# Kernel tuning notes

Measured on AMD Instinct MI355X. Metric: run time of the kernel, lower is better.

Reference implementation:

```python
import jax, jax.numpy as jnp
import numpy as np

TEMP = 1.0
EPS = 1e-6


def trop_linear(x, w, b, temp=TEMP):
    # x: (..., in), w: (out, in) -> (..., out)
    # y_i = temp * logsumexp_j((w_ij + x_j)/temp) + b_i  (soft tropical / max-plus)
    z = x[..., None, :] + w  # (..., out, in)
    y = temp * jax.nn.logsumexp(z / temp, axis=-1)
    return y + b


def trop_layernorm(x, weight, bias, eps=EPS):
    n = x.shape[-1]
    # torch.median returns the lower of the two middle elements for even n
    med = jnp.sort(x, axis=-1)[..., (n - 1) // 2][..., None]
    q75 = jnp.quantile(x, 0.75, axis=-1, keepdims=True)
    q25 = jnp.quantile(x, 0.25, axis=-1, keepdims=True)
    iqr = jnp.maximum(q75 - q25, eps)
    return (x - med) / iqr * weight + bias


def setup_inputs() -> dict:
    key = jax.random.key(0)
    ks = jax.random.split(key, 8)
    B, D_IN, D_H, D_OUT = 1024, 512, 512, 256
    return {
        "x": jax.random.normal(ks[0], (B, D_IN), dtype=jnp.float32),
        "w1": 0.1 * jax.random.normal(ks[1], (D_H, D_IN), dtype=jnp.float32),
        "b1": jnp.zeros((D_H,), dtype=jnp.float32),
        "ln1_w": jnp.ones((D_H,), dtype=jnp.float32),
        "ln1_b": jnp.zeros((D_H,), dtype=jnp.float32),
        "w2": 0.1 * jax.random.normal(ks[2], (D_H, D_H), dtype=jnp.float32),
        "b2": jnp.zeros((D_H,), dtype=jnp.float32),
        "ln2_w": jnp.ones((D_H,), dtype=jnp.float32),
        "ln2_b": jnp.zeros((D_H,), dtype=jnp.float32),
        "w3": 0.1 * jax.random.normal(ks[3], (D_OUT, D_H), dtype=jnp.float32),
        "b3": jnp.zeros((D_OUT,), dtype=jnp.float32),
    }


def reference(x, w1, b1, ln1_w, ln1_b, w2, b2, ln2_w, ln2_b, w3, b3):
    h = trop_linear(x, w1, b1)
    h = trop_layernorm(h, ln1_w, ln1_b)
    h = jnp.maximum(h, 0.0)  # TropicalActivation('relu', threshold=0)
    h = trop_linear(h, w2, b2)
    h = trop_layernorm(h, ln2_w, ln2_b)
    h = jnp.maximum(h, 0.0)
    return trop_linear(h, w3, b3)
```

## Files before the change

kernel.cpp:

```cpp
#include <hip/hip_runtime.h>
#include <math.h>


typedef float v4f __attribute__((ext_vector_type(4)));

#define ELS_B 528
#define LN64f 4.1588830833596715f

__device__ __forceinline__ int pk4_fp8(float a, float b, float c, float d) {
    int p = __builtin_amdgcn_cvt_pk_fp8_f32(a, b, 0, 0);
    p = __builtin_amdgcn_cvt_pk_fp8_f32(c, d, p, 1);
    return p;
}

__global__ __launch_bounds__(256) void expW_frag(const float* __restrict__ w1,
                                                 const float* __restrict__ w2,
                                                 const float* __restrict__ w3,
                                                 uint8_t* __restrict__ Ef) {
    int u = blockIdx.x * 256 + threadIdx.x;
    int lane = u & 63, t = (u >> 6) & 15, S = u >> 10;
    int r = lane & 15, q = lane >> 4;
    const float* w; int tile;
    if (S < 32)      { w = w1; tile = S; }
    else if (S < 64) { w = w2; tile = S - 32; }
    else             { w = w3; tile = S - 64; }
    const float* src = w + (tile * 16 + r) * 512 + t * 32 + q * 8;
    float4 a = *reinterpret_cast<const float4*>(src);
    float4 b = *reinterpret_cast<const float4*>(src + 4);
    int2 o;
    o.x = pk4_fp8(__expf(a.x), __expf(a.y), __expf(a.z), __expf(a.w));
    o.y = pk4_fp8(__expf(b.x), __expf(b.y), __expf(b.z), __expf(b.w));
    *reinterpret_cast<int2*>(Ef + u * 8) = o;
}

__device__ __forceinline__ void load_areg(const uint8_t* Els, int lane, long* areg) {
    const uint8_t* ap = Els + (lane & 1) * ELS_B + ((lane >> 4) & 3) * 8;
#pragma unroll
    for (int t = 0; t < 16; ++t)
        areg[t] = *reinterpret_cast<const long*>(ap + t * 32);
}

template <int NSUB>
__device__ __forceinline__ void prefetchB(const uint8_t* __restrict__ bp,
                                          int s0, long bb[8][4]) {
#pragma unroll
    for (int p = 0; p < 8; ++p)
#pragma unroll
        for (int s = 0; s < NSUB; ++s)
            bb[p][s] = *reinterpret_cast<const long*>(bp + ((s0 + s) * 16 + p) * 512);
}

template <int NSUB>
__device__ __forceinline__ void gemm_body(const uint8_t* __restrict__ bp,
                                          int s0, const long* areg,
                                          long bb[8][4], v4f* acc) {
#pragma unroll
    for (int s = 0; s < NSUB; ++s) acc[s] = (v4f){0.f, 0.f, 0.f, 0.f};
#pragma unroll
    for (int t = 0; t < 16; ++t) {
        long a = areg[t];
        long bcur[NSUB];
#pragma unroll
        for (int s = 0; s < NSUB; ++s) bcur[s] = bb[t & 7][s];
        if (t < 8) {
#pragma unroll
            for (int s = 0; s < NSUB; ++s)
                bb[t & 7][s] =
                    *reinterpret_cast<const long*>(bp + ((s0 + s) * 16 + t + 8) * 512);
        }
#pragma unroll
        for (int s = 0; s < NSUB; ++s)
            acc[s] = __builtin_amdgcn_mfma_f32_16x16x32_fp8_fp8(a, bcur[s],
                                                                acc[s], 0, 0, 0);
    }
}

__device__ __forceinline__ void sort_shuf(float& v0, float& v1, int lane,
                                          int ebase, int k, int jjhi) {
#pragma clang loop unroll(disable)
    for (int jj = jjhi; jj >= 2; jj >>= 1) {
        int lm = jj >> 1;
        bool keepmin = (((ebase & k) == 0) == ((lane & lm) == 0));
        float p0 = __shfl_xor(v0, lm);
        float p1 = __shfl_xor(v1, lm);
        v0 = keepmin ? fminf(v0, p0) : fmaxf(v0, p0);
        v1 = keepmin ? fminf(v1, p1) : fmaxf(v1, p1);
    }
    bool up = ((ebase & k) == 0);
    float lo = fminf(v0, v1), hi = fmaxf(v0, v1);
    v0 = up ? lo : hi;
    v1 = up ? hi : lo;
}

__device__ __forceinline__ void ln_row4(float* hb,
                                        const float* __restrict__ lw,
                                        const float* __restrict__ lb,
                                        uint8_t* Els_row, float* crow_row,
                                        float* cmx_row,
                                        int W, int lane) {
    const int e0 = W * 128 + lane * 2;
    float2 lwv = *reinterpret_cast<const float2*>(lw + e0);
    float2 lbv = *reinterpret_cast<const float2*>(lb + e0);
    float2 hv = *reinterpret_cast<const float2*>(hb + e0);
    float h0 = hv.x, h1 = hv.y, v0 = h0, v1 = h1;

#pragma clang loop unroll(disable)
    for (int k = 2; k <= 128; k <<= 1)
        sort_shuf(v0, v1, lane, e0, k, (k >> 1) > 64 ? 64 : (k >> 1));

    __syncthreads();
    *reinterpret_cast<float2*>(hb + e0) = make_float2(v0, v1);
    __syncthreads();
    {
        bool keepmin = (((e0 & 256) == 0) == ((e0 & 128) == 0));
        float2 p = *reinterpret_cast<const float2*>(hb + (e0 ^ 128));
        v0 = keepmin ? fminf(v0, p.x) : fmaxf(v0, p.x);
        v1 = keepmin ? fminf(v1, p.y) : fmaxf(v1, p.y);
    }
    sort_shuf(v0, v1, lane, e0, 256, 64);

    __syncthreads();
    *reinterpret_cast<float2*>(hb + e0) = make_float2(v0, v1);
    __syncthreads();
    {
        bool keepmin = ((e0 & 256) == 0);
        float2 p = *reinterpret_cast<const float2*>(hb + (e0 ^ 256));
        v0 = keepmin ? fminf(v0, p.x) : fmaxf(v0, p.x);
        v1 = keepmin ? fminf(v1, p.y) : fmaxf(v1, p.y);
    }
    __syncthreads();
    *reinterpret_cast<float2*>(hb + e0) = make_float2(v0, v1);
    __syncthreads();
    {
        bool keepmin = ((e0 & 128) == 0);
        float2 p = *reinterpret_cast<const float2*>(hb + (e0 ^ 128));
        v0 = keepmin ? fminf(v0, p.x) : fmaxf(v0, p.x);
        v1 = keepmin ? fminf(v1, p.y) : fmaxf(v1, p.y);
    }
    sort_shuf(v0, v1, lane, e0, 512, 64);

    __syncthreads();
    *reinterpret_cast<float2*>(hb + e0) = make_float2(v0, v1);
    __syncthreads();
    float s127 = hb[127], s128 = hb[128], med = hb[255];
    float s383 = hb[383], s384 = hb[384];
    float q25 = s127 + 0.75f * (s128 - s127);
    float q75 = s383 + 0.25f * (s384 - s383);
    float inv = 1.0f / fmaxf(q75 - q25, 1e-6f);

    float y0 = fmaxf((h0 - med) * inv * lwv.x + lbv.x, 0.0f);
    float y1 = fmaxf((h1 - med) * inv * lwv.y + lbv.y, 0.0f);
    float cm = fmaxf(y0, y1);
#pragma unroll
    for (int s = 32; s > 0; s >>= 1) cm = fmaxf(cm, __shfl_xor(cm, s));
    if (lane == 0) cmx_row[W] = cm;
    __syncthreads();
    cm = fmaxf(fmaxf(cmx_row[0], cmx_row[1]), fmaxf(cmx_row[2], cmx_row[3]));

    int p = __builtin_amdgcn_cvt_pk_fp8_f32(64.0f * __expf(y0 - cm),
                                            64.0f * __expf(y1 - cm), 0, 0);
    *reinterpret_cast<ushort*>(Els_row + e0) = (ushort)p;
    if (lane == 0 && W == 0) crow_row[0] = cm;
}

__global__ __launch_bounds__(512, 4) void fused_rows(
    const float* __restrict__ x,
    const float* __restrict__ b1,
    const float* __restrict__ ln1w, const float* __restrict__ ln1b,
    const float* __restrict__ b2,
    const float* __restrict__ ln2w, const float* __restrict__ ln2b,
    const float* __restrict__ b3,
    const uint8_t* __restrict__ Ew,
    float* __restrict__ out)
{
    __shared__ uint8_t Els[2 * ELS_B];
    __shared__ float hbuf[2 * 512];
    __shared__ float crow[2];
    __shared__ float cmx[2][4];

    const int tid = threadIdx.x;
    const int lane = tid & 63;
    const int w = tid >> 6;
    const int r = lane & 15, q = lane >> 4;
    const int row = w >> 2, W = w & 3;
    const int blk = blockIdx.x;

    const uint8_t* bp1 = Ew + lane * 8;
    const uint8_t* bp2 = bp1 + 262144;
    const uint8_t* bp3 = bp1 + 524288;

    long bb[8][4];
    long areg[16];
    v4f acc[4];

    prefetchB<4>(bp1, w * 4, bb);

    if (tid < 256) {
        int rr = tid >> 7, col = (tid & 127) * 4;
        float4 a = *reinterpret_cast<const float4*>(x + blk * 1024 + rr * 512 + col);
        *reinterpret_cast<int*>(&Els[rr * ELS_B + col]) =
            pk4_fp8(4.0f * __expf(a.x), 4.0f * __expf(a.y),
                    4.0f * __expf(a.z), 4.0f * __expf(a.w));
    }
    __syncthreads();

    load_areg(Els, lane, areg);
    gemm_body<4>(bp1, w * 4, areg, bb, acc);
    {
        v4f av = (q == 0) ? acc[0] : (q == 1) ? acc[1] : (q == 2) ? acc[2] : acc[3];
        int col = (w * 4 + q) * 16 + r;
        float bbv = b1[col];
        hbuf[col]       = __logf(av[0]) + bbv;
        hbuf[512 + col] = __logf(av[1]) + bbv;
    }
    prefetchB<4>(bp2, w * 4, bb);
    __syncthreads();
    ln_row4(hbuf + row * 512, ln1w, ln1b, Els + row * ELS_B,
            crow + row, cmx[row], W, lane);
    __syncthreads();

    load_areg(Els, lane, areg);
    gemm_body<4>(bp2, w * 4, areg, bb, acc);
    {
        v4f av = (q == 0) ? acc[0] : (q == 1) ? acc[1] : (q == 2) ? acc[2] : acc[3];
        int col = (w * 4 + q) * 16 + r;
        float bbv = b2[col];
        hbuf[col]       = __logf(av[0]) + bbv;
        hbuf[512 + col] = __logf(av[1]) + bbv;
    }
    prefetchB<2>(bp3, w * 2, bb);
    __syncthreads();
    ln_row4(hbuf + row * 512, ln2w, ln2b, Els + row * ELS_B,
            crow + row, cmx[row], W, lane);
    __syncthreads();

    load_areg(Els, lane, areg);
    gemm_body<2>(bp3, w * 2, areg, bb, acc);
    if (q < 2) {
        v4f av = (q == 0) ? acc[0] : acc[1];
        int col = (w * 2 + q) * 16 + r;
        float bbv = b3[col] - LN64f;
        out[(blk * 2 + 0) * 256 + col] = __logf(av[0]) + crow[0] + bbv;
        out[(blk * 2 + 1) * 256 + col] = __logf(av[1]) + crow[1] + bbv;
    }
}

extern "C" void kernel_launch(void* const* d_in, const int* in_sizes, int n_in,
                              void* d_out, int out_size, void* d_ws, size_t ws_size,
                              hipStream_t stream) {
    const float* x    = (const float*)d_in[0];
    const float* w1   = (const float*)d_in[1];
    const float* b1   = (const float*)d_in[2];
    const float* ln1w = (const float*)d_in[3];
    const float* ln1b = (const float*)d_in[4];
    const float* w2   = (const float*)d_in[5];
    const float* b2   = (const float*)d_in[6];
    const float* ln2w = (const float*)d_in[7];
    const float* ln2b = (const float*)d_in[8];
    const float* w3   = (const float*)d_in[9];
    const float* b3   = (const float*)d_in[10];
    float* out = (float*)d_out;

    uint8_t* Ew = (uint8_t*)d_ws;

    expW_frag<<<320, 256, 0, stream>>>(w1, w2, w3, Ew);
    fused_rows<<<512, 512, 0, stream>>>(x, b1, ln1w, ln1b, b2, ln2w, ln2b,
                                        b3, Ew, out);
}
```

Before: 105.1 us.

## Process one row per block with all 8 waves cooperating on the sort

Each block now handles a single batch row instead of two, so the grid doubles to 1024 blocks and all eight waves sort one 512-element row with one element per lane. The bitonic sort moves from 2-per-lane shuffles plus LDS exchanges to a 1-per-lane network, with more barrier-synchronised LDS stages for strides of 64 and up. Launch bounds are raised to target 8 blocks per CU. The MFMA A operand now uses only one real row, so half of each fp8 matmul's work is wasted, and every weight fragment is fetched twice as often across the grid.

```diff
diff --git a/kernel.cpp b/kernel.cpp
--- a/kernel.cpp
+++ b/kernel.cpp
@@ -34,7 +34,7 @@
 }
 
 __device__ __forceinline__ void load_areg(const uint8_t* Els, int lane, long* areg) {
-    const uint8_t* ap = Els + (lane & 1) * ELS_B + ((lane >> 4) & 3) * 8;
+    const uint8_t* ap = Els + ((lane >> 4) & 3) * 8;
 #pragma unroll
     for (int t = 0; t < 16; ++t)
         areg[t] = *reinterpret_cast<const long*>(ap + t * 32);
@@ -75,72 +75,46 @@
     }
 }
 
-__device__ __forceinline__ void sort_shuf(float& v0, float& v1, int lane,
-                                          int ebase, int k, int jjhi) {
-#pragma clang loop unroll(disable)
-    for (int jj = jjhi; jj >= 2; jj >>= 1) {
-        int lm = jj >> 1;
-        bool keepmin = (((ebase & k) == 0) == ((lane & lm) == 0));
-        float p0 = __shfl_xor(v0, lm);
-        float p1 = __shfl_xor(v1, lm);
-        v0 = keepmin ? fminf(v0, p0) : fmaxf(v0, p0);
-        v1 = keepmin ? fminf(v1, p1) : fmaxf(v1, p1);
-    }
-    bool up = ((ebase & k) == 0);
-    float lo = fminf(v0, v1), hi = fmaxf(v0, v1);
-    v0 = up ? lo : hi;
-    v1 = up ? hi : lo;
-}
-
-__device__ __forceinline__ void ln_row4(float* hb,
+__device__ __forceinline__ void ln_row8(float* hb,
                                         const float* __restrict__ lw,
                                         const float* __restrict__ lb,
-                                        uint8_t* Els_row, float* crow_row,
-                                        float* cmx_row,
-                                        int W, int lane) {
-    const int e0 = W * 128 + lane * 2;
-    float2 lwv = *reinterpret_cast<const float2*>(lw + e0);
-    float2 lbv = *reinterpret_cast<const float2*>(lb + e0);
-    float2 hv = *reinterpret_cast<const float2*>(hb + e0);
-    float h0 = hv.x, h1 = hv.y, v0 = h0, v1 = h1;
-
-#pragma clang loop unroll(disable)
-    for (int k = 2; k <= 128; k <<= 1)
-        sort_shuf(v0, v1, lane, e0, k, (k >> 1) > 64 ? 64 : (k >> 1));
-
-    __syncthreads();
-    *reinterpret_cast<float2*>(hb + e0) = make_float2(v0, v1);
-    __syncthreads();
-    {
-        bool keepmin = (((e0 & 256) == 0) == ((e0 & 128) == 0));
-        float2 p = *reinterpret_cast<const float2*>(hb + (e0 ^ 128));
-        v0 = keepmin ? fminf(v0, p.x) : fmaxf(v0, p.x);
-        v1 = keepmin ? fminf(v1, p.y) : fmaxf(v1, p.y);
-    }
-    sort_shuf(v0, v1, lane, e0, 256, 64);
-
-    __syncthreads();
-    *reinterpret_cast<float2*>(hb + e0) = make_float2(v0, v1);
-    __syncthreads();
-    {
-        bool keepmin = ((e0 & 256) == 0);
-        float2 p = *reinterpret_cast<const float2*>(hb + (e0 ^ 256));
-        v0 = keepmin ? fminf(v0, p.x) : fmaxf(v0, p.x);
-        v1 = keepmin ? fminf(v1, p.y) : fmaxf(v1, p.y);
-    }
-    __syncthreads();
-    *reinterpret_cast<float2*>(hb + e0) = make_float2(v0, v1);
-    __syncthreads();
-    {
-        bool keepmin = ((e0 & 128) == 0);
-        float2 p = *reinterpret_cast<const float2*>(hb + (e0 ^ 128));
-        v0 = keepmin ? fminf(v0, p.x) : fmaxf(v0, p.x);
-        v1 = keepmin ? fminf(v1, p.y) : fmaxf(v1, p.y);
-    }
-    sort_shuf(v0, v1, lane, e0, 512, 64);
-
-    __syncthreads();
-    *reinterpret_cast<float2*>(hb + e0) = make_float2(v0, v1);
+                                        uint8_t* Els, float* crow,
+                                        float* cmx,
+                                        int w, int lane) {
+    const int e = w * 64 + lane;
+    float lwv = lw[e], lbv = lb[e];
+    float h = hb[e];
+    float v = h;
+
+#pragma clang loop unroll(disable)
+    for (int k = 2; k <= 64; k <<= 1) {
+#pragma clang loop unroll(disable)
+        for (int jj = (k >> 1); jj >= 1; jj >>= 1) {
+            float p = __shfl_xor(v, jj);
+            bool keepmin = (((e & k) == 0) == ((lane & jj) == 0));
+            v = keepmin ? fminf(v, p) : fmaxf(v, p);
+        }
+    }
+#pragma clang loop unroll(disable)
+    for (int k = 128; k <= 512; k <<= 1) {
+#pragma clang loop unroll(disable)
+        for (int jj = (k >> 1); jj >= 64; jj >>= 1) {
+            __syncthreads();
+            hb[e] = v;
+            __syncthreads();
+            float p = hb[e ^ jj];
+            bool keepmin = (((e & k) == 0) == ((e & jj) == 0));
+            v = keepmin ? fminf(v, p) : fmaxf(v, p);
+        }
+#pragma clang loop unroll(disable)
+        for (int jj = 32; jj >= 1; jj >>= 1) {
+            float p = __shfl_xor(v, jj);
+            bool keepmin = (((e & k) == 0) == ((lane & jj) == 0));
+            v = keepmin ? fminf(v, p) : fmaxf(v, p);
+        }
+    }
+    __syncthreads();
+    hb[e] = v;
     __syncthreads();
     float s127 = hb[127], s128 = hb[128], med = hb[255];
     float s383 = hb[383], s384 = hb[384];
@@ -148,22 +122,21 @@
     float q75 = s383 + 0.25f * (s384 - s383);
     float inv = 1.0f / fmaxf(q75 - q25, 1e-6f);
 
-    float y0 = fmaxf((h0 - med) * inv * lwv.x + lbv.x, 0.0f);
-    float y1 = fmaxf((h1 - med) * inv * lwv.y + lbv.y, 0.0f);
-    float cm = fmaxf(y0, y1);
+    float y = fmaxf((h - med) * inv * lwv + lbv, 0.0f);
+    float cm = y;
 #pragma unroll
     for (int s = 32; s > 0; s >>= 1) cm = fmaxf(cm, __shfl_xor(cm, s));
-    if (lane == 0) cmx_row[W] = cm;
-    __syncthreads();
-    cm = fmaxf(fmaxf(cmx_row[0], cmx_row[1]), fmaxf(cmx_row[2], cmx_row[3]));
-
-    int p = __builtin_amdgcn_cvt_pk_fp8_f32(64.0f * __expf(y0 - cm),
-                                            64.0f * __expf(y1 - cm), 0, 0);
-    *reinterpret_cast<ushort*>(Els_row + e0) = (ushort)p;
-    if (lane == 0 && W == 0) crow_row[0] = cm;
-}
-
-__global__ __launch_bounds__(512, 4) void fused_rows(
+    if (lane == 0) cmx[w] = cm;
+    __syncthreads();
+    cm = fmaxf(fmaxf(fmaxf(cmx[0], cmx[1]), fmaxf(cmx[2], cmx[3])),
+               fmaxf(fmaxf(cmx[4], cmx[5]), fmaxf(cmx[6], cmx[7])));
+
+    int p = __builtin_amdgcn_cvt_pk_fp8_f32(64.0f * __expf(y - cm), 0.0f, 0, 0);
+    Els[e] = (uint8_t)(p & 0xff);
+    if (w == 0 && lane == 0) crow[0] = cm;
+}
+
+__global__ __launch_bounds__(512, 8) void fused_rows(
     const float* __restrict__ x,
     const float* __restrict__ b1,
     const float* __restrict__ ln1w, const float* __restrict__ ln1b,
@@ -173,16 +146,15 @@
     const uint8_t* __restrict__ Ew,
     float* __restrict__ out)
 {
-    __shared__ uint8_t Els[2 * ELS_B];
-    __shared__ float hbuf[2 * 512];
-    __shared__ float crow[2];
-    __shared__ float cmx[2][4];
+    __shared__ uint8_t Els[ELS_B];
+    __shared__ float hbuf[512];
+    __shared__ float crow[1];
+    __shared__ float cmx[8];
 
     const int tid = threadIdx.x;
     const int lane = tid & 63;
     const int w = tid >> 6;
     const int r = lane & 15, q = lane >> 4;
-    const int row = w >> 2, W = w & 3;
     const int blk = blockIdx.x;
 
     const uint8_t* bp1 = Ew + lane * 8;
@@ -195,10 +167,10 @@
 
     prefetchB<4>(bp1, w * 4, bb);
 
-    if (tid < 256) {
-        int rr = tid >> 7, col = (tid & 127) * 4;
-        float4 a = *reinterpret_cast<const float4*>(x + blk * 1024 + rr * 512 + col);
-        *reinterpret_cast<int*>(&Els[rr * ELS_B + col]) =
+    if (tid < 128) {
+        int col = tid * 4;
+        float4 a = *reinterpret_cast<const float4*>(x + blk * 512 + col);
+        *reinterpret_cast<int*>(&Els[col]) =
             pk4_fp8(4.0f * __expf(a.x), 4.0f * __expf(a.y),
                     4.0f * __expf(a.z), 4.0f * __expf(a.w));
     }
@@ -209,14 +181,11 @@
     {
         v4f av = (q == 0) ? acc[0] : (q == 1) ? acc[1] : (q == 2) ? acc[2] : acc[3];
         int col = (w * 4 + q) * 16 + r;
-        float bbv = b1[col];
-        hbuf[col]       = __logf(av[0]) + bbv;
-        hbuf[512 + col] = __logf(av[1]) + bbv;
+        hbuf[col] = __logf(av[0]) + b1[col];
     }
     prefetchB<4>(bp2, w * 4, bb);
     __syncthreads();
-    ln_row4(hbuf + row * 512, ln1w, ln1b, Els + row * ELS_B,
-            crow + row, cmx[row], W, lane);
+    ln_row8(hbuf, ln1w, ln1b, Els, crow, cmx, w, lane);
     __syncthreads();
 
     load_areg(Els, lane, areg);
@@ -224,14 +193,11 @@
     {
         v4f av = (q == 0) ? acc[0] : (q == 1) ? acc[1] : (q == 2) ? acc[2] : acc[3];
         int col = (w * 4 + q) * 16 + r;
-        float bbv = b2[col];
-        hbuf[col]       = __logf(av[0]) + bbv;
-        hbuf[512 + col] = __logf(av[1]) + bbv;
+        hbuf[col] = __logf(av[0]) + b2[col];
     }
     prefetchB<2>(bp3, w * 2, bb);
     __syncthreads();
-    ln_row4(hbuf + row * 512, ln2w, ln2b, Els + row * ELS_B,
-            crow + row, cmx[row], W, lane);
+    ln_row8(hbuf, ln2w, ln2b, Els, crow, cmx, w, lane);
     __syncthreads();
 
     load_areg(Els, lane, areg);
@@ -239,9 +205,7 @@
     if (q < 2) {
         v4f av = (q == 0) ? acc[0] : acc[1];
         int col = (w * 2 + q) * 16 + r;
-        float bbv = b3[col] - LN64f;
-        out[(blk * 2 + 0) * 256 + col] = __logf(av[0]) + crow[0] + bbv;
-        out[(blk * 2 + 1) * 256 + col] = __logf(av[1]) + crow[1] + bbv;
+        out[blk * 256 + col] = __logf(av[0]) + crow[0] + b3[col] - LN64f;
     }
 }
 
@@ -264,6 +228,6 @@
     uint8_t* Ew = (uint8_t*)d_ws;
 
     expW_frag<<<320, 256, 0, stream>>>(w1, w2, w3, Ew);
-    fused_rows<<<512, 512, 0, stream>>>(x, b1, ln1w, ln1b, b2, ln2w, ln2b,
-                                        b3, Ew, out);
-}
+    fused_rows<<<1024, 512, 0, stream>>>(x, b1, ln1w, ln1b, b2, ln2w, ln2b,
+                                         b3, Ew, out);
+}
```

Result: slower. 167.9 us (+59.7%).

## Process one row per 256-thread block and shrink B prefetch to double buffer

Applied to the files above, without the earlier changes.

The fused kernel now handles one batch row per block with 4 waves, instead of two rows per 512-thread block with 8 waves. Each wave now covers 8 output subtiles instead of 4, and the weight fragment prefetch shrinks from an 8-deep register buffer to a 2-deep ping-pong issued after each MFMA step. This drops the per-row layernorm split across wave groups and should lower register pressure and raise occupancy with smaller blocks. In exchange each block reads the full weight set for only one row, which halves weight reuse, and the shallower prefetch may expose more global load latency.

```diff
diff --git a/kernel.cpp b/kernel.cpp
--- a/kernel.cpp
+++ b/kernel.cpp
@@ -4,7 +4,6 @@
 
 typedef float v4f __attribute__((ext_vector_type(4)));
 
-#define ELS_B 528
 #define LN64f 4.1588830833596715f
 
 __device__ __forceinline__ int pk4_fp8(float a, float b, float c, float d) {
@@ -33,45 +32,42 @@
     *reinterpret_cast<int2*>(Ef + u * 8) = o;
 }
 
-__device__ __forceinline__ void load_areg(const uint8_t* Els, int lane, long* areg) {
-    const uint8_t* ap = Els + (lane & 1) * ELS_B + ((lane >> 4) & 3) * 8;
+__device__ __forceinline__ void load_areg(const uint8_t* Els, int q, long* areg) {
+    const uint8_t* ap = Els + q * 8;
 #pragma unroll
     for (int t = 0; t < 16; ++t)
         areg[t] = *reinterpret_cast<const long*>(ap + t * 32);
 }
 
 template <int NSUB>
-__device__ __forceinline__ void prefetchB(const uint8_t* __restrict__ bp,
-                                          int s0, long bb[8][4]) {
-#pragma unroll
-    for (int p = 0; p < 8; ++p)
+__device__ __forceinline__ void prefetchB2(const uint8_t* __restrict__ bp,
+                                           int s0, long bb[2][NSUB]) {
+#pragma unroll
+    for (int p = 0; p < 2; ++p)
 #pragma unroll
         for (int s = 0; s < NSUB; ++s)
             bb[p][s] = *reinterpret_cast<const long*>(bp + ((s0 + s) * 16 + p) * 512);
 }
 
 template <int NSUB>
-__device__ __forceinline__ void gemm_body(const uint8_t* __restrict__ bp,
-                                          int s0, const long* areg,
-                                          long bb[8][4], v4f* acc) {
+__device__ __forceinline__ void gemm_body2(const uint8_t* __restrict__ bp,
+                                           int s0, const long* areg,
+                                           long bb[2][NSUB], v4f* acc) {
 #pragma unroll
     for (int s = 0; s < NSUB; ++s) acc[s] = (v4f){0.f, 0.f, 0.f, 0.f};
 #pragma unroll
     for (int t = 0; t < 16; ++t) {
         long a = areg[t];
-        long bcur[NSUB];
-#pragma unroll
-        for (int s = 0; s < NSUB; ++s) bcur[s] = bb[t & 7][s];
-        if (t < 8) {
+#pragma unroll
+        for (int s = 0; s < NSUB; ++s)
+            acc[s] = __builtin_amdgcn_mfma_f32_16x16x32_fp8_fp8(a, bb[t & 1][s],
+                                                                acc[s], 0, 0, 0);
+        if (t < 14) {
 #pragma unroll
             for (int s = 0; s < NSUB; ++s)
-                bb[t & 7][s] =
-                    *reinterpret_cast<const long*>(bp + ((s0 + s) * 16 + t + 8) * 512);
+                bb[t & 1][s] =
+                    *reinterpret_cast<const long*>(bp + ((s0 + s) * 16 + t + 2) * 512);
         }
-#pragma unroll
-        for (int s = 0; s < NSUB; ++s)
-            acc[s] = __builtin_amdgcn_mfma_f32_16x16x32_fp8_fp8(a, bcur[s],
-                                                                acc[s], 0, 0, 0);
     }
 }
 
@@ -163,7 +159,7 @@
     if (lane == 0 && W == 0) crow_row[0] = cm;
 }
 
-__global__ __launch_bounds__(512, 4) void fused_rows(
+__global__ __launch_bounds__(256) void fused_rows(
     const float* __restrict__ x,
     const float* __restrict__ b1,
     const float* __restrict__ ln1w, const float* __restrict__ ln1b,
@@ -173,75 +169,71 @@
     const uint8_t* __restrict__ Ew,
     float* __restrict__ out)
 {
-    __shared__ uint8_t Els[2 * ELS_B];
-    __shared__ float hbuf[2 * 512];
-    __shared__ float crow[2];
-    __shared__ float cmx[2][4];
+    __shared__ uint8_t Els[512];
+    __shared__ float hbuf[512];
+    __shared__ float crow[1];
+    __shared__ float cmx[4];
 
     const int tid = threadIdx.x;
     const int lane = tid & 63;
     const int w = tid >> 6;
     const int r = lane & 15, q = lane >> 4;
-    const int row = w >> 2, W = w & 3;
     const int blk = blockIdx.x;
 
     const uint8_t* bp1 = Ew + lane * 8;
     const uint8_t* bp2 = bp1 + 262144;
     const uint8_t* bp3 = bp1 + 524288;
 
-    long bb[8][4];
+    long bb[2][8];
+    long bb3[2][4];
     long areg[16];
-    v4f acc[4];
-
-    prefetchB<4>(bp1, w * 4, bb);
-
-    if (tid < 256) {
-        int rr = tid >> 7, col = (tid & 127) * 4;
-        float4 a = *reinterpret_cast<const float4*>(x + blk * 1024 + rr * 512 + col);
-        *reinterpret_cast<int*>(&Els[rr * ELS_B + col]) =
-            pk4_fp8(4.0f * __expf(a.x), 4.0f * __expf(a.y),
-                    4.0f * __expf(a.z), 4.0f * __expf(a.w));
-    }
-    __syncthreads();
-
-    load_areg(Els, lane, areg);
-    gemm_body<4>(bp1, w * 4, areg, bb, acc);
+    v4f acc[8];
+
+    prefetchB2<8>(bp1, w * 8, bb);
+
+    {
+        int col = tid * 2;
+        float2 a = *reinterpret_cast<const float2*>(x + blk * 512 + col);
+        int p = __builtin_amdgcn_cvt_pk_fp8_f32(4.0f * __expf(a.x),
+                                                4.0f * __expf(a.y), 0, 0);
+        *reinterpret_cast<ushort*>(&Els[col]) = (ushort)p;
+    }
+    __syncthreads();
+
+    load_areg(Els, q, areg);
+    gemm_body2<8>(bp1, w * 8, areg, bb, acc);
+    {
+        v4f a0 = (q == 0) ? acc[0] : (q == 1) ? acc[2] : (q == 2) ? acc[4] : acc[6];
+        v4f a1 = (q == 0) ? acc[1] : (q == 1) ? acc[3] : (q == 2) ? acc[5] : acc[7];
+        int c0 = (w * 8 + 2 * q) * 16 + r, c1 = c0 + 16;
+        hbuf[c0] = __logf(a0[0]) + b1[c0];
+        hbuf[c1] = __logf(a1[0]) + b1[c1];
+    }
+    prefetchB2<8>(bp2, w * 8, bb);
+    __syncthreads();
+    ln_row4(hbuf, ln1w, ln1b, Els, crow, cmx, w, lane);
+    __syncthreads();
+
+    load_areg(Els, q, areg);
+    gemm_body2<8>(bp2, w * 8, areg, bb, acc);
+    {
+        v4f a0 = (q == 0) ? acc[0] : (q == 1) ? acc[2] : (q == 2) ? acc[4] : acc[6];
+        v4f a1 = (q == 0) ? acc[1] : (q == 1) ? acc[3] : (q == 2) ? acc[5] : acc[7];
+        int c0 = (w * 8 + 2 * q) * 16 + r, c1 = c0 + 16;
+        hbuf[c0] = __logf(a0[0]) + b2[c0];
+        hbuf[c1] = __logf(a1[0]) + b2[c1];
+    }
+    prefetchB2<4>(bp3, w * 4, bb3);
+    __syncthreads();
+    ln_row4(hbuf, ln2w, ln2b, Els, crow, cmx, w, lane);
+    __syncthreads();
+
+    load_areg(Els, q, areg);
+    gemm_body2<4>(bp3, w * 4, areg, bb3, acc);
     {
         v4f av = (q == 0) ? acc[0] : (q == 1) ? acc[1] : (q == 2) ? acc[2] : acc[3];
         int col = (w * 4 + q) * 16 + r;
-        float bbv = b1[col];
-        hbuf[col]       = __logf(av[0]) + bbv;
-        hbuf[512 + col] = __logf(av[1]) + bbv;
-    }
-    prefetchB<4>(bp2, w * 4, bb);
-    __syncthreads();
-    ln_row4(hbuf + row * 512, ln1w, ln1b, Els + row * ELS_B,
-            crow + row, cmx[row], W, lane);
-    __syncthreads();
-
-    load_areg(Els, lane, areg);
-    gemm_body<4>(bp2, w * 4, areg, bb, acc);
-    {
-        v4f av = (q == 0) ? acc[0] : (q == 1) ? acc[1] : (q == 2) ? acc[2] : acc[3];
-        int col = (w * 4 + q) * 16 + r;
-        float bbv = b2[col];
-        hbuf[col]       = __logf(av[0]) + bbv;
-        hbuf[512 + col] = __logf(av[1]) + bbv;
-    }
-    prefetchB<2>(bp3, w * 2, bb);
-    __syncthreads();
-    ln_row4(hbuf + row * 512, ln2w, ln2b, Els + row * ELS_B,
-            crow + row, cmx[row], W, lane);
-    __syncthreads();
-
-    load_areg(Els, lane, areg);
-    gemm_body<2>(bp3, w * 2, areg, bb, acc);
-    if (q < 2) {
-        v4f av = (q == 0) ? acc[0] : acc[1];
-        int col = (w * 2 + q) * 16 + r;
-        float bbv = b3[col] - LN64f;
-        out[(blk * 2 + 0) * 256 + col] = __logf(av[0]) + crow[0] + bbv;
-        out[(blk * 2 + 1) * 256 + col] = __logf(av[1]) + crow[1] + bbv;
+        out[blk * 256 + col] = __logf(av[0]) + crow[0] + b3[col] - LN64f;
     }
 }
 
@@ -264,6 +256,6 @@
     uint8_t* Ew = (uint8_t*)d_ws;
 
     expW_frag<<<320, 256, 0, stream>>>(w1, w2, w3, Ew);
-    fused_rows<<<512, 512, 0, stream>>>(x, b1, ln1w, ln1b, b2, ln2w, ln2b,
-                                        b3, Ew, out);
-}
+    fused_rows<<<1024, 256, 0, stream>>>(x, b1, ln1w, ln1b, b2, ln2w, ln2b,
+                                         b3, Ew, out);
+}
```

After: 122.6 us. 16.6% more time.
